# Optimization experiments

Hardware: AMD Instinct MI355X
Metric: run time of the kernel (lower is better)

Reference implementation:

```python
import jax, jax.numpy as jnp
import numpy as np

NEG_SLOPE = 0.01  # torch nn.LeakyReLU default
N_NODES = 100000
N_EDGES = 500000
IN_DIM, OUT_DIM, EF_DIM, EMB_DIM = 128, 128, 64, 256


def leaky_relu(x):
    return jnp.where(x >= 0, x, NEG_SLOPE * x)


def setup_inputs() -> dict:
    key = jax.random.key(0)
    ks = jax.random.split(key, 8)
    s = 0.05
    nf = jax.random.normal(ks[0], (N_NODES, IN_DIM), dtype=jnp.float32)
    ef = jax.random.normal(ks[1], (N_EDGES, EF_DIM), dtype=jnp.float32)
    src = jax.random.randint(ks[2], (N_EDGES,), 0, N_NODES, dtype=jnp.int32)
    dst = jax.random.randint(ks[3], (N_EDGES,), 0, N_NODES, dtype=jnp.int32)
    # Linear weights stored as (in, out); y = x @ W. No biases (bias=False).
    We1 = jax.random.normal(ks[4], (2 * IN_DIM + EF_DIM, EMB_DIM), dtype=jnp.float32) * s
    We2 = jax.random.normal(ks[5], (EMB_DIM, OUT_DIM), dtype=jnp.float32) * s
    Wn1 = jax.random.normal(ks[6], (IN_DIM + OUT_DIM, EMB_DIM), dtype=jnp.float32) * s
    Wn2 = jax.random.normal(ks[7], (EMB_DIM, OUT_DIM), dtype=jnp.float32) * s
    return {"nf": nf, "ef": ef, "src": src, "dst": dst,
            "We1": We1, "We2": We2, "Wn1": Wn1, "Wn2": Wn2}


def reference(nf, ef, src, dst, We1, We2, Wn1, Wn2):
    # Symmetrize: add reversed edges carrying the same edge features.
    src_full = jnp.concatenate([src, dst])            # [2E]
    dst_full = jnp.concatenate([dst, src])            # [2E]
    ef_full = jnp.concatenate([ef, ef], axis=0)       # [2E, ef_dim]

    # message_func: MLP over [src_nf | dst_nf | ef]
    edge_in = jnp.concatenate([nf[src_full], nf[dst_full], ef_full], axis=-1)  # [2E, 2*in+ef]
    msg = leaky_relu(edge_in @ We1) @ We2              # [2E, out]

    # reduce_func: sum messages per destination node (zeros for isolated nodes)
    red = jax.ops.segment_sum(msg, dst_full, num_segments=nf.shape[0])  # [N, out]

    # apply_node_func: MLP over [nf | red_msg]
    node_in = jnp.concatenate([nf, red], axis=-1)      # [N, in+out]
    out_nf = leaky_relu(node_in @ Wn1) @ Wn2           # [N, out]
    return out_nf
```

## Files before the change

### kernel.cpp

```cpp
#include <hip/hip_runtime.h>
#include <hip/hip_bf16.h>
#include <string.h>


using f32x4  = __attribute__((ext_vector_type(4))) float;
using bf16x8 = __attribute__((ext_vector_type(8))) short;

#define LROW 72
#define CROW 132

__device__ __forceinline__ float lrelu(float x) { return x >= 0.f ? x : 0.01f * x; }

__device__ __forceinline__ ushort f2bf(float f) {
    union { float f; unsigned u; } v; v.f = f;
    unsigned u = v.u;
    return (ushort)((u + 0x7fffu + ((u >> 16) & 1u)) >> 16);
}
__device__ __forceinline__ float bf2f(ushort u) {
    union { unsigned u; float f; } v; v.u = ((unsigned)u) << 16; return v.f;
}

__device__ __forceinline__ void atomic_pk_add_bf16(void* addr, unsigned val) {
    asm volatile("global_atomic_pk_add_bf16 %0, %1, off" : : "v"(addr), "v"(val) : "memory");
}

__global__ __launch_bounds__(256) void gemm_bf16(
    const ushort* __restrict__ X1, int K1,
    const ushort* __restrict__ X2, int K2,
    const ushort* __restrict__ Wt,
    void* __restrict__ out, int Nw, int Mstore, int flags)
{
    __shared__ ushort Xs[128 * LROW];
    __shared__ ushort Ws[128 * LROW];

    const int K    = K1 + K2;
    const int tid  = threadIdx.x;
    const int lane = tid & 63;
    const int wv   = tid >> 6;
    const int wm   = wv >> 1, wn = wv & 1;
    const int row0 = blockIdx.x * 128;
    const int col0 = blockIdx.y * 128;

    f32x4 acc[4][4] = {};

    for (int k0 = 0; k0 < K; k0 += 64) {
        const ushort* Xsrc; int kloc, ksz;
        if (k0 < K1) { Xsrc = X1; kloc = k0;      ksz = K1; }
        else         { Xsrc = X2; kloc = k0 - K1; ksz = K2; }

        const int r_  = tid >> 3;
        const int kk  = (tid & 7) * 8;
        uint4 xv[4], wvv[4];
        #pragma unroll
        for (int p = 0; p < 4; ++p) {
            int r = p * 32 + r_;
            xv[p]  = *reinterpret_cast<const uint4*>(Xsrc + (size_t)(row0 + r) * ksz + kloc + kk);
            wvv[p] = *reinterpret_cast<const uint4*>(Wt   + (size_t)(col0 + r) * K   + k0   + kk);
        }
        __syncthreads();
        #pragma unroll
        for (int p = 0; p < 4; ++p) {
            int r = p * 32 + r_;
            *reinterpret_cast<uint4*>(&Xs[r * LROW + kk]) = xv[p];
            *reinterpret_cast<uint4*>(&Ws[r * LROW + kk]) = wvv[p];
        }
        __syncthreads();

        #pragma unroll
        for (int ks = 0; ks < 2; ++ks) {
            bf16x8 af[4], bfr[4];
            #pragma unroll
            for (int i = 0; i < 4; ++i) {
                int mrow = wm * 64 + i * 16 + (lane & 15);
                af[i]  = *reinterpret_cast<const bf16x8*>(&Xs[mrow * LROW + ks * 32 + (lane >> 4) * 8]);
                int ncol = wn * 64 + i * 16 + (lane & 15);
                bfr[i] = *reinterpret_cast<const bf16x8*>(&Ws[ncol * LROW + ks * 32 + (lane >> 4) * 8]);
            }
            #pragma unroll
            for (int i = 0; i < 4; ++i)
                #pragma unroll
                for (int j = 0; j < 4; ++j)
                    acc[i][j] = __builtin_amdgcn_mfma_f32_16x16x32_bf16(af[i], bfr[j], acc[i][j], 0, 0, 0);
        }
    }

    #pragma unroll
    for (int i = 0; i < 4; ++i) {
        int gr0 = row0 + wm * 64 + i * 16 + ((lane >> 4) << 2);
        #pragma unroll
        for (int j = 0; j < 4; ++j) {
            int gc = col0 + wn * 64 + j * 16 + (lane & 15);
            #pragma unroll
            for (int r = 0; r < 4; ++r) {
                int gr = gr0 + r;
                if (gr >= Mstore) continue;
                float v = acc[i][j][r];
                if (flags & 1) v = lrelu(v);
                if (flags & 2) ((ushort*)out)[(size_t)gr * Nw + gc] = f2bf(v);
                else           ((float*) out)[(size_t)gr * Nw + gc] = v;
            }
        }
    }
}

__global__ __launch_bounds__(256) void edge_fused(
    const ushort* __restrict__ efb,
    const ushort* __restrict__ Wet,
    const ushort* __restrict__ AB,
    const int* __restrict__ src, const int* __restrict__ dst,
    ushort* __restrict__ H,
    int E)
{
    __shared__ ushort lds[128 * LROW * 2];
    __shared__ int sd[256];

    const int tid  = threadIdx.x;
    const int lane = tid & 63;
    const int wv   = tid >> 6;
    const int wm   = wv >> 1, wn = wv & 1;
    const int bid  = blockIdx.x;
    const int eb   = (bid >> 1) * 128;
    const int col0 = (bid & 1) * 128;

    ushort* Xs = lds;
    ushort* Ws = lds + 128 * LROW;

    const int r_ = tid >> 3;
    const int kk = (tid & 7) * 8;
    uint4 xv[4], wvv[4];
    #pragma unroll
    for (int p = 0; p < 4; ++p) {
        int r = p * 32 + r_;
        xv[p]  = *reinterpret_cast<const uint4*>(efb + (size_t)(eb + r) * 64 + kk);
        wvv[p] = *reinterpret_cast<const uint4*>(Wet + (size_t)(col0 + r) * 64 + kk);
    }
    if (tid < 128) sd[tid] = (eb + tid < E)         ? src[eb + tid]         : -1;
    else           sd[tid] = (eb + (tid - 128) < E) ? dst[eb + (tid - 128)] : -1;
    #pragma unroll
    for (int p = 0; p < 4; ++p) {
        int r = p * 32 + r_;
        *reinterpret_cast<uint4*>(&Xs[r * LROW + kk]) = xv[p];
        *reinterpret_cast<uint4*>(&Ws[r * LROW + kk]) = wvv[p];
    }
    __syncthreads();

    f32x4 acc[4][4] = {};
    #pragma unroll
    for (int ks = 0; ks < 2; ++ks) {
        bf16x8 af[4], bfr[4];
        #pragma unroll
        for (int i = 0; i < 4; ++i) {
            int mrow = wm * 64 + i * 16 + (lane & 15);
            af[i]  = *reinterpret_cast<const bf16x8*>(&Xs[mrow * LROW + ks * 32 + (lane >> 4) * 8]);
            int ncol = wn * 64 + i * 16 + (lane & 15);
            bfr[i] = *reinterpret_cast<const bf16x8*>(&Ws[ncol * LROW + ks * 32 + (lane >> 4) * 8]);
        }
        #pragma unroll
        for (int i = 0; i < 4; ++i)
            #pragma unroll
            for (int j = 0; j < 4; ++j)
                acc[i][j] = __builtin_amdgcn_mfma_f32_16x16x32_bf16(af[i], bfr[j], acc[i][j], 0, 0, 0);
    }
    __syncthreads();

    ushort* Cs = lds;
    #pragma unroll
    for (int i = 0; i < 4; ++i) {
        int er0 = wm * 64 + i * 16 + ((lane >> 4) << 2);
        #pragma unroll
        for (int j = 0; j < 4; ++j) {
            int fc = wn * 64 + j * 16 + (lane & 15);
            #pragma unroll
            for (int r = 0; r < 4; ++r)
                Cs[(er0 + r) * CROW + fc] = f2bf(acc[i][j][r]);
        }
    }
    __syncthreads();

    const int jj = lane * 2;
    const ushort* ABj = AB + col0 + jj;
    ushort* Hj = H + col0 + jj;
    for (int p = 0; p < 32; ++p) {
        int ee = p * 4 + wv;
        int s = sd[ee], d = sd[128 + ee];
        if (s < 0) continue;
        ushort2 cv = *(const ushort2*)(&Cs[ee * CROW + jj]);
        ushort2 as = *(const ushort2*)(ABj + (size_t)s * 512);
        ushort2 bs = *(const ushort2*)(ABj + (size_t)s * 512 + 256);
        ushort2 ad = *(const ushort2*)(ABj + (size_t)d * 512);
        ushort2 bd = *(const ushort2*)(ABj + (size_t)d * 512 + 256);
        float c0 = bf2f(cv.x), c1 = bf2f(cv.y);
        ushort2 mf, mb;
        mf.x = f2bf(lrelu(bf2f(as.x) + bf2f(bd.x) + c0));
        mf.y = f2bf(lrelu(bf2f(as.y) + bf2f(bd.y) + c1));
        mb.x = f2bf(lrelu(bf2f(ad.x) + bf2f(bs.x) + c0));
        mb.y = f2bf(lrelu(bf2f(ad.y) + bf2f(bs.y) + c1));
        unsigned uf, ub;
        memcpy(&uf, &mf, 4); memcpy(&ub, &mb, 4);
        atomic_pk_add_bf16(Hj + (size_t)d * 256, uf);
        atomic_pk_add_bf16(Hj + (size_t)s * 256, ub);
    }
}

__global__ __launch_bounds__(256) void cvt_pad(
    const float* __restrict__ x, ushort* __restrict__ y, size_t n_real, size_t n_pad)
{
    size_t i = ((size_t)blockIdx.x * 256 + threadIdx.x) * 4;
    if (i >= n_pad) return;
    ushort4 o;
    if (i < n_real) {
        float4 v = *(const float4*)(x + i);
        o.x = f2bf(v.x); o.y = f2bf(v.y); o.z = f2bf(v.z); o.w = f2bf(v.w);
    } else { o.x = 0; o.y = 0; o.z = 0; o.w = 0; }
    *(ushort4*)(y + i) = o;
}

__global__ __launch_bounds__(256) void wcvt(
    const float* __restrict__ We1, const float* __restrict__ We2,
    const float* __restrict__ Wn1, const float* __restrict__ Wn2,
    ushort* __restrict__ Wabt, ushort* __restrict__ Wet, ushort* __restrict__ We2t,
    ushort* __restrict__ Wn1t, ushort* __restrict__ Wn2t)
{
    int idx = blockIdx.x * 256 + threadIdx.x;
    switch (blockIdx.y) {
    case 0: if (idx < 256*128) { int n = idx >> 7, k = idx & 127; Wabt[idx]            = f2bf(We1[k * 256 + n]); } break;
    case 1: if (idx < 256*128) { int n = idx >> 7, k = idx & 127; Wabt[32768 + idx]    = f2bf(We1[(128 + k) * 256 + n]); } break;
    case 2: if (idx < 256*64)  { int n = idx >> 6, k = idx & 63;  Wet[idx]             = f2bf(We1[(256 + k) * 256 + n]); } break;
    case 3: if (idx < 128*256) { int n = idx >> 8, k = idx & 255; We2t[idx]            = f2bf(We2[k * 128 + n]); } break;
    case 4: if (idx < 256*256) { int n = idx >> 8, k = idx & 255; Wn1t[idx]            = f2bf(Wn1[k * 256 + n]); } break;
    case 5: if (idx < 128*256) { int n = idx >> 8, k = idx & 255; Wn2t[idx]            = f2bf(Wn2[k * 128 + n]); } break;
    }
}

extern "C" void kernel_launch(void* const* d_in, const int* in_sizes, int n_in,
                              void* d_out, int out_size, void* d_ws, size_t ws_size,
                              hipStream_t stream) {
    const float* nf  = (const float*)d_in[0];
    const float* ef  = (const float*)d_in[1];
    const int*   src = (const int*)d_in[2];
    const int*   dst = (const int*)d_in[3];
    const float* We1 = (const float*)d_in[4];
    const float* We2 = (const float*)d_in[5];
    const float* Wn1 = (const float*)d_in[6];
    const float* Wn2 = (const float*)d_in[7];
    float* out = (float*)d_out;

    const int  N  = in_sizes[0] / 128;
    const int  E  = in_sizes[2];
    const int  Np = (N + 127) & ~127;
    const long Ep = ((long)E + 127) & ~127L;

    char* p = (char*)d_ws;
    auto alloc = [&](size_t bytes) { char* r = p; p += (bytes + 255) & ~(size_t)255; return r; };
    ushort* AB   = (ushort*)alloc((size_t)Np * 512 * 2);
    ushort* H    = (ushort*)alloc((size_t)Np * 256 * 2);
    ushort* nfb  = (ushort*)alloc((size_t)Np * 128 * 2);
    ushort* efb  = (ushort*)alloc((size_t)Ep * 64 * 2);
    ushort* Wabt = (ushort*)alloc(65536 * 2);
    ushort* Wet  = (ushort*)alloc(16384 * 2);
    ushort* We2t = (ushort*)alloc(32768 * 2);
    ushort* Wn1t = (ushort*)alloc(65536 * 2);
    ushort* Wn2t = (ushort*)alloc(32768 * 2);
    ushort* red = AB;
    ushort* hid = AB + (size_t)Np * 128;

    dim3 blk(256);

    wcvt<<<dim3(256, 6), blk, 0, stream>>>(We1, We2, Wn1, Wn2, Wabt, Wet, We2t, Wn1t, Wn2t);
    cvt_pad<<<dim3((unsigned)((size_t)Np * 128 / 1024)), blk, 0, stream>>>(nf, nfb, (size_t)N * 128, (size_t)Np * 128);
    cvt_pad<<<dim3((unsigned)((size_t)Ep * 64 / 1024)), blk, 0, stream>>>(ef, efb, (size_t)E * 64, (size_t)Ep * 64);

    gemm_bf16<<<dim3(Np / 128, 4), blk, 0, stream>>>(nfb, 128, nullptr, 0, Wabt, AB, 512, Np, 2);

    hipMemsetAsync(H, 0, (size_t)Np * 256 * 2, stream);

    edge_fused<<<dim3((unsigned)(Ep / 128 * 2)), blk, 0, stream>>>(
        efb, Wet, AB, src, dst, H, E);

    gemm_bf16<<<dim3(Np / 128, 1), blk, 0, stream>>>(H, 256, nullptr, 0, We2t, red, 128, Np, 2);
    gemm_bf16<<<dim3(Np / 128, 2), blk, 0, stream>>>(nfb, 128, red, 128, Wn1t, hid, 256, Np, 2 | 1);
    gemm_bf16<<<dim3(Np / 128, 1), blk, 0, stream>>>(hid, 256, nullptr, 0, Wn2t, (void*)out, 128, N, 0);
}
```

Before: 962.2 us.

## Bucket edges by destination node block and reduce messages in LDS

Replaces the per-edge kernel that scattered bf16 packed atomics into global H with a binning pass (count, scan, scatter) that groups directed edges by 64-node destination block. A new kernel then processes each block's edges, computes the edge-feature GEMM per bucket, accumulates messages in fp32 shared memory, and writes H once, removing the global memset and atomics. The cost is extra binning kernels with global atomics, a single-block scan, and a duplicated edge-feature GEMM across both directions. Per-bucket work is also uneven, and the edge-feature rows are now gathered straight from global memory.

```diff
diff --git a/kernel.cpp b/kernel.cpp
--- a/kernel.cpp
+++ b/kernel.cpp
@@ -8,6 +8,8 @@
 
 #define LROW 72
 #define CROW 132
+#define BSH  6
+#define BNODES 64
 
 __device__ __forceinline__ float lrelu(float x) { return x >= 0.f ? x : 0.01f * x; }
 
@@ -18,10 +20,6 @@
 }
 __device__ __forceinline__ float bf2f(ushort u) {
     union { unsigned u; float f; } v; v.u = ((unsigned)u) << 16; return v.f;
-}
-
-__device__ __forceinline__ void atomic_pk_add_bf16(void* addr, unsigned val) {
-    asm volatile("global_atomic_pk_add_bf16 %0, %1, off" : : "v"(addr), "v"(val) : "memory");
 }
 
 __global__ __launch_bounds__(256) void gemm_bf16(
@@ -103,102 +101,162 @@
     }
 }
 
-__global__ __launch_bounds__(256) void edge_fused(
+__global__ __launch_bounds__(256) void ebin_count(
+    const int* __restrict__ src, const int* __restrict__ dst,
+    int* __restrict__ cnt, int E, int NB)
+{
+    int i = blockIdx.x * 256 + threadIdx.x;
+    if (i >= E) return;
+    atomicAdd(&cnt[dst[i] >> BSH], 1);
+    atomicAdd(&cnt[NB + (src[i] >> BSH)], 1);
+}
+
+__global__ __launch_bounds__(256) void escan(
+    const int* __restrict__ cnt, int* __restrict__ base, int* __restrict__ cur, int n)
+{
+    __shared__ int ps[256];
+    const int t = threadIdx.x;
+    const int per = (n + 255) / 256;
+    int s = 0;
+    for (int i = 0; i < per; ++i) { int idx = t * per + i; if (idx < n) s += cnt[idx]; }
+    ps[t] = s;
+    __syncthreads();
+    for (int off = 1; off < 256; off <<= 1) {
+        int u = (t >= off) ? ps[t - off] : 0;
+        __syncthreads();
+        ps[t] += u;
+        __syncthreads();
+    }
+    int run = ps[t] - s;
+    for (int i = 0; i < per; ++i) {
+        int idx = t * per + i;
+        if (idx < n) { base[idx] = run; cur[idx] = run; run += cnt[idx]; }
+    }
+    if (t == 255) base[n] = run;
+}
+
+__global__ __launch_bounds__(256) void escatter(
+    const int* __restrict__ src, const int* __restrict__ dst,
+    int* __restrict__ cur, int* __restrict__ perm, int E, int NB)
+{
+    int i = blockIdx.x * 256 + threadIdx.x;
+    if (i >= E) return;
+    int p1 = atomicAdd(&cur[dst[i] >> BSH], 1);       perm[p1] = i;
+    int p2 = atomicAdd(&cur[NB + (src[i] >> BSH)], 1); perm[p2] = i;
+}
+
+__global__ __launch_bounds__(512) void edge_bucket(
     const ushort* __restrict__ efb,
     const ushort* __restrict__ Wet,
     const ushort* __restrict__ AB,
     const int* __restrict__ src, const int* __restrict__ dst,
+    const int* __restrict__ perm, const int* __restrict__ base,
     ushort* __restrict__ H,
-    int E)
-{
-    __shared__ ushort lds[128 * LROW * 2];
-    __shared__ int sd[256];
-
-    const int tid  = threadIdx.x;
-    const int lane = tid & 63;
-    const int wv   = tid >> 6;
-    const int wm   = wv >> 1, wn = wv & 1;
-    const int bid  = blockIdx.x;
-    const int eb   = (bid >> 1) * 128;
-    const int col0 = (bid & 1) * 128;
-
-    ushort* Xs = lds;
-    ushort* Ws = lds + 128 * LROW;
-
-    const int r_ = tid >> 3;
-    const int kk = (tid & 7) * 8;
-    uint4 xv[4], wvv[4];
+    int NB)
+{
+    __shared__ ushort Ws[128 * LROW];
+    __shared__ ushort Cs[BNODES * CROW];
+    __shared__ float  Hs[BNODES * 128];
+    __shared__ int eids[64], ownl[64], othn[64];
+
+    const int tid   = threadIdx.x;
+    const int lane  = tid & 63;
+    const int wv    = tid >> 6;
+    const int wm    = wv >> 1, wn = wv & 1;
+    const int b     = blockIdx.x;
+    const int col0  = blockIdx.y * 128;
+    const int node0 = b << BSH;
+
     #pragma unroll
-    for (int p = 0; p < 4; ++p) {
-        int r = p * 32 + r_;
-        xv[p]  = *reinterpret_cast<const uint4*>(efb + (size_t)(eb + r) * 64 + kk);
-        wvv[p] = *reinterpret_cast<const uint4*>(Wet + (size_t)(col0 + r) * 64 + kk);
-    }
-    if (tid < 128) sd[tid] = (eb + tid < E)         ? src[eb + tid]         : -1;
-    else           sd[tid] = (eb + (tid - 128) < E) ? dst[eb + (tid - 128)] : -1;
-    #pragma unroll
-    for (int p = 0; p < 4; ++p) {
-        int r = p * 32 + r_;
-        *reinterpret_cast<uint4*>(&Xs[r * LROW + kk]) = xv[p];
-        *reinterpret_cast<uint4*>(&Ws[r * LROW + kk]) = wvv[p];
+    for (int i = 0; i < 16; ++i) Hs[tid + i * 512] = 0.f;
+
+    {
+        const int r_ = tid >> 3;
+        const int kk = (tid & 7) * 8;
+        #pragma unroll
+        for (int p = 0; p < 2; ++p) {
+            int r = p * 64 + r_;
+            *reinterpret_cast<uint4*>(&Ws[r * LROW + kk]) =
+                *reinterpret_cast<const uint4*>(Wet + (size_t)(col0 + r) * 64 + kk);
+        }
+    }
+
+    const int d0 = base[b],      d1 = base[b + 1];
+    const int s0 = base[NB + b], s1 = base[NB + b + 1];
+    const int cd = d1 - d0;
+    const int nv = cd + (s1 - s0);
+
+    for (int v0 = 0; v0 < nv; v0 += 64) {
+        __syncthreads();
+        if (tid < 64) {
+            int vid = v0 + tid;
+            int e = 0, own = -1, oth = 0;
+            if (vid < nv) {
+                if (vid < cd) { e = perm[d0 + vid];      own = dst[e]; oth = src[e]; }
+                else          { e = perm[s0 + vid - cd]; own = src[e]; oth = dst[e]; }
+            }
+            eids[tid] = e;
+            ownl[tid] = (own < 0) ? -1 : own - node0;
+            othn[tid] = oth;
+        }
+        __syncthreads();
+
+        f32x4 acc[4] = {};
+        #pragma unroll
+        for (int ks = 0; ks < 2; ++ks) {
+            int mrow = wm * 16 + (lane & 15);
+            int e = eids[mrow];
+            bf16x8 af = *reinterpret_cast<const bf16x8*>(
+                efb + (size_t)e * 64 + ks * 32 + (lane >> 4) * 8);
+            #pragma unroll
+            for (int j = 0; j < 4; ++j) {
+                int ncol = wn * 64 + j * 16 + (lane & 15);
+                bf16x8 bf = *reinterpret_cast<const bf16x8*>(
+                    &Ws[ncol * LROW + ks * 32 + (lane >> 4) * 8]);
+                acc[j] = __builtin_amdgcn_mfma_f32_16x16x32_bf16(af, bf, acc[j], 0, 0, 0);
+            }
+        }
+        {
+            int er0 = wm * 16 + ((lane >> 4) << 2);
+            #pragma unroll
+            for (int j = 0; j < 4; ++j) {
+                int fc = wn * 64 + j * 16 + (lane & 15);
+                #pragma unroll
+                for (int r = 0; r < 4; ++r)
+                    Cs[(er0 + r) * CROW + fc] = f2bf(acc[j][r]);
+            }
+        }
+        __syncthreads();
+
+        const int jj = lane * 2;
+        #pragma unroll
+        for (int p = 0; p < 8; ++p) {
+            int v = p * 8 + wv;
+            int ol = ownl[v];
+            float w = (ol >= 0) ? 1.f : 0.f;
+            ol &= (BNODES - 1);
+            int oth = othn[v];
+            ushort2 av = *(const ushort2*)(AB + (size_t)oth * 512 + col0 + jj);
+            ushort2 bv = *(const ushort2*)(AB + (size_t)(node0 + ol) * 512 + 256 + col0 + jj);
+            ushort2 cv = *(const ushort2*)(&Cs[v * CROW + jj]);
+            float m0 = lrelu(bf2f(av.x) + bf2f(bv.x) + bf2f(cv.x));
+            float m1 = lrelu(bf2f(av.y) + bf2f(bv.y) + bf2f(cv.y));
+            atomicAdd(&Hs[ol * 128 + jj],     w * m0);
+            atomicAdd(&Hs[ol * 128 + jj + 1], w * m1);
+        }
     }
     __syncthreads();
 
-    f32x4 acc[4][4] = {};
-    #pragma unroll
-    for (int ks = 0; ks < 2; ++ks) {
-        bf16x8 af[4], bfr[4];
-        #pragma unroll
-        for (int i = 0; i < 4; ++i) {
-            int mrow = wm * 64 + i * 16 + (lane & 15);
-            af[i]  = *reinterpret_cast<const bf16x8*>(&Xs[mrow * LROW + ks * 32 + (lane >> 4) * 8]);
-            int ncol = wn * 64 + i * 16 + (lane & 15);
-            bfr[i] = *reinterpret_cast<const bf16x8*>(&Ws[ncol * LROW + ks * 32 + (lane >> 4) * 8]);
-        }
-        #pragma unroll
-        for (int i = 0; i < 4; ++i)
-            #pragma unroll
-            for (int j = 0; j < 4; ++j)
-                acc[i][j] = __builtin_amdgcn_mfma_f32_16x16x32_bf16(af[i], bfr[j], acc[i][j], 0, 0, 0);
-    }
-    __syncthreads();
-
-    ushort* Cs = lds;
-    #pragma unroll
-    for (int i = 0; i < 4; ++i) {
-        int er0 = wm * 64 + i * 16 + ((lane >> 4) << 2);
-        #pragma unroll
-        for (int j = 0; j < 4; ++j) {
-            int fc = wn * 64 + j * 16 + (lane & 15);
-            #pragma unroll
-            for (int r = 0; r < 4; ++r)
-                Cs[(er0 + r) * CROW + fc] = f2bf(acc[i][j][r]);
-        }
-    }
-    __syncthreads();
-
-    const int jj = lane * 2;
-    const ushort* ABj = AB + col0 + jj;
-    ushort* Hj = H + col0 + jj;
-    for (int p = 0; p < 32; ++p) {
-        int ee = p * 4 + wv;
-        int s = sd[ee], d = sd[128 + ee];
-        if (s < 0) continue;
-        ushort2 cv = *(const ushort2*)(&Cs[ee * CROW + jj]);
-        ushort2 as = *(const ushort2*)(ABj + (size_t)s * 512);
-        ushort2 bs = *(const ushort2*)(ABj + (size_t)s * 512 + 256);
-        ushort2 ad = *(const ushort2*)(ABj + (size_t)d * 512);
-        ushort2 bd = *(const ushort2*)(ABj + (size_t)d * 512 + 256);
-        float c0 = bf2f(cv.x), c1 = bf2f(cv.y);
-        ushort2 mf, mb;
-        mf.x = f2bf(lrelu(bf2f(as.x) + bf2f(bd.x) + c0));
-        mf.y = f2bf(lrelu(bf2f(as.y) + bf2f(bd.y) + c1));
-        mb.x = f2bf(lrelu(bf2f(ad.x) + bf2f(bs.x) + c0));
-        mb.y = f2bf(lrelu(bf2f(ad.y) + bf2f(bs.y) + c1));
-        unsigned uf, ub;
-        memcpy(&uf, &mf, 4); memcpy(&ub, &mb, 4);
-        atomic_pk_add_bf16(Hj + (size_t)d * 256, uf);
-        atomic_pk_add_bf16(Hj + (size_t)s * 256, ub);
+    {
+        int row = tid >> 3, seg = tid & 7;
+        ushort* dp = H + (size_t)(node0 + row) * 256 + col0 + seg * 16;
+        #pragma unroll
+        for (int q = 0; q < 8; ++q) {
+            ushort2 o;
+            o.x = f2bf(Hs[row * 128 + seg * 16 + q * 2]);
+            o.y = f2bf(Hs[row * 128 + seg * 16 + q * 2 + 1]);
+            *(ushort2*)(dp + q * 2) = o;
+        }
     }
 }
 
@@ -249,33 +307,42 @@
     const int  E  = in_sizes[2];
     const int  Np = (N + 127) & ~127;
     const long Ep = ((long)E + 127) & ~127L;
+    const int  NB = Np >> BSH;
 
     char* p = (char*)d_ws;
     auto alloc = [&](size_t bytes) { char* r = p; p += (bytes + 255) & ~(size_t)255; return r; };
-    ushort* AB   = (ushort*)alloc((size_t)Np * 512 * 2);
-    ushort* H    = (ushort*)alloc((size_t)Np * 256 * 2);
-    ushort* nfb  = (ushort*)alloc((size_t)Np * 128 * 2);
-    ushort* efb  = (ushort*)alloc((size_t)Ep * 64 * 2);
-    ushort* Wabt = (ushort*)alloc(65536 * 2);
-    ushort* Wet  = (ushort*)alloc(16384 * 2);
-    ushort* We2t = (ushort*)alloc(32768 * 2);
-    ushort* Wn1t = (ushort*)alloc(65536 * 2);
-    ushort* Wn2t = (ushort*)alloc(32768 * 2);
+    ushort* AB    = (ushort*)alloc((size_t)Np * 512 * 2);
+    ushort* H     = (ushort*)alloc((size_t)Np * 256 * 2);
+    ushort* nfb   = (ushort*)alloc((size_t)Np * 128 * 2);
+    ushort* efb   = (ushort*)alloc((size_t)Ep * 64 * 2);
+    ushort* Wabt  = (ushort*)alloc(65536 * 2);
+    ushort* Wet   = (ushort*)alloc(16384 * 2);
+    ushort* We2t  = (ushort*)alloc(32768 * 2);
+    ushort* Wn1t  = (ushort*)alloc(65536 * 2);
+    ushort* Wn2t  = (ushort*)alloc(32768 * 2);
+    int*    cnt   = (int*)alloc((size_t)(2 * NB) * 4);
+    int*    basep = (int*)alloc((size_t)(2 * NB + 1) * 4);
+    int*    cur   = (int*)alloc((size_t)(2 * NB) * 4);
+    int*    perm  = (int*)alloc((size_t)2 * E * 4);
     ushort* red = AB;
     ushort* hid = AB + (size_t)Np * 128;
 
     dim3 blk(256);
+    const unsigned egrid = (unsigned)((E + 255) / 256);
 
     wcvt<<<dim3(256, 6), blk, 0, stream>>>(We1, We2, Wn1, Wn2, Wabt, Wet, We2t, Wn1t, Wn2t);
     cvt_pad<<<dim3((unsigned)((size_t)Np * 128 / 1024)), blk, 0, stream>>>(nf, nfb, (size_t)N * 128, (size_t)Np * 128);
     cvt_pad<<<dim3((unsigned)((size_t)Ep * 64 / 1024)), blk, 0, stream>>>(ef, efb, (size_t)E * 64, (size_t)Ep * 64);
 
+    hipMemsetAsync(cnt, 0, (size_t)(2 * NB) * 4, stream);
+    ebin_count<<<dim3(egrid), blk, 0, stream>>>(src, dst, cnt, E, NB);
+    escan<<<dim3(1), blk, 0, stream>>>(cnt, basep, cur, 2 * NB);
+    escatter<<<dim3(egrid), blk, 0, stream>>>(src, dst, cur, perm, E, NB);
+
     gemm_bf16<<<dim3(Np / 128, 4), blk, 0, stream>>>(nfb, 128, nullptr, 0, Wabt, AB, 512, Np, 2);
 
-    hipMemsetAsync(H, 0, (size_t)Np * 256 * 2, stream);
-
-    edge_fused<<<dim3((unsigned)(Ep / 128 * 2)), blk, 0, stream>>>(
-        efb, Wet, AB, src, dst, H, E);
+    edge_bucket<<<dim3(NB, 2), dim3(512), 0, stream>>>(
+        efb, Wet, AB, src, dst, perm, basep, H, NB);
 
     gemm_bf16<<<dim3(Np / 128, 1), blk, 0, stream>>>(H, 256, nullptr, 0, We2t, red, 128, Np, 2);
     gemm_bf16<<<dim3(Np / 128, 2), blk, 0, stream>>>(nfb, 128, red, 128, Wn1t, hid, 256, Np, 2 | 1);
```

Measured after the change: 2.319 ms. 2.41x slower.

## Fuse node-side GEMM chain into one kernel and specialize AB projection GEMM

Applied to the files above, without the earlier changes.

Replaces the three node-side GEMM launches (H·We2, [nf|red]·Wn1 with leaky ReLU, hid·Wn2) with a single per-row-tile kernel. The kernel keeps the reduced messages and hidden activations in LDS instead of writing them to global memory and reading them back. The AB projection GEMM now loads the node tile into LDS once and loops over all four column blocks, reading weights directly from global memory (likely L2-resident) rather than staging them. The cost is high register and LDS use per block, which may lower occupancy, plus uncoalesced weight reads from global memory.

```diff
diff --git a/kernel.cpp b/kernel.cpp
--- a/kernel.cpp
+++ b/kernel.cpp
@@ -8,6 +8,8 @@
 
 #define LROW 72
 #define CROW 132
+#define P128 132
+#define P256 264
 
 __device__ __forceinline__ float lrelu(float x) { return x >= 0.f ? x : 0.01f * x; }
 
@@ -24,80 +26,55 @@
     asm volatile("global_atomic_pk_add_bf16 %0, %1, off" : : "v"(addr), "v"(val) : "memory");
 }
 
-__global__ __launch_bounds__(256) void gemm_bf16(
-    const ushort* __restrict__ X1, int K1,
-    const ushort* __restrict__ X2, int K2,
+__global__ __launch_bounds__(256) void gemm_ab(
+    const ushort* __restrict__ X,
     const ushort* __restrict__ Wt,
-    void* __restrict__ out, int Nw, int Mstore, int flags)
+    ushort* __restrict__ out)
 {
-    __shared__ ushort Xs[128 * LROW];
-    __shared__ ushort Ws[128 * LROW];
-
-    const int K    = K1 + K2;
+    __shared__ ushort Xs[128 * P128];
     const int tid  = threadIdx.x;
     const int lane = tid & 63;
     const int wv   = tid >> 6;
     const int wm   = wv >> 1, wn = wv & 1;
     const int row0 = blockIdx.x * 128;
-    const int col0 = blockIdx.y * 128;
-
-    f32x4 acc[4][4] = {};
-
-    for (int k0 = 0; k0 < K; k0 += 64) {
-        const ushort* Xsrc; int kloc, ksz;
-        if (k0 < K1) { Xsrc = X1; kloc = k0;      ksz = K1; }
-        else         { Xsrc = X2; kloc = k0 - K1; ksz = K2; }
-
-        const int r_  = tid >> 3;
-        const int kk  = (tid & 7) * 8;
-        uint4 xv[4], wvv[4];
-        #pragma unroll
-        for (int p = 0; p < 4; ++p) {
-            int r = p * 32 + r_;
-            xv[p]  = *reinterpret_cast<const uint4*>(Xsrc + (size_t)(row0 + r) * ksz + kloc + kk);
-            wvv[p] = *reinterpret_cast<const uint4*>(Wt   + (size_t)(col0 + r) * K   + k0   + kk);
-        }
-        __syncthreads();
-        #pragma unroll
-        for (int p = 0; p < 4; ++p) {
-            int r = p * 32 + r_;
-            *reinterpret_cast<uint4*>(&Xs[r * LROW + kk]) = xv[p];
-            *reinterpret_cast<uint4*>(&Ws[r * LROW + kk]) = wvv[p];
-        }
-        __syncthreads();
-
-        #pragma unroll
-        for (int ks = 0; ks < 2; ++ks) {
-            bf16x8 af[4], bfr[4];
+
+    #pragma unroll
+    for (int q = 0; q < 8; ++q) {
+        int idx = q * 256 + tid;
+        int r = idx >> 4, c = idx & 15;
+        *reinterpret_cast<uint4*>(&Xs[r * P128 + c * 8]) =
+            *reinterpret_cast<const uint4*>(X + (size_t)(row0 + r) * 128 + c * 8);
+    }
+    __syncthreads();
+
+    const int g8 = (lane >> 4) * 8;
+    for (int cb = 0; cb < 4; ++cb) {
+        f32x4 acc[4][4] = {};
+        #pragma unroll
+        for (int ks = 0; ks < 4; ++ks) {
+            bf16x8 af[4], bf[4];
             #pragma unroll
             for (int i = 0; i < 4; ++i) {
                 int mrow = wm * 64 + i * 16 + (lane & 15);
-                af[i]  = *reinterpret_cast<const bf16x8*>(&Xs[mrow * LROW + ks * 32 + (lane >> 4) * 8]);
-                int ncol = wn * 64 + i * 16 + (lane & 15);
-                bfr[i] = *reinterpret_cast<const bf16x8*>(&Ws[ncol * LROW + ks * 32 + (lane >> 4) * 8]);
+                af[i] = *reinterpret_cast<const bf16x8*>(&Xs[mrow * P128 + ks * 32 + g8]);
+                int nc = cb * 128 + wn * 64 + i * 16 + (lane & 15);
+                bf[i] = *reinterpret_cast<const bf16x8*>(Wt + (size_t)nc * 128 + ks * 32 + g8);
             }
             #pragma unroll
             for (int i = 0; i < 4; ++i)
                 #pragma unroll
                 for (int j = 0; j < 4; ++j)
-                    acc[i][j] = __builtin_amdgcn_mfma_f32_16x16x32_bf16(af[i], bfr[j], acc[i][j], 0, 0, 0);
-        }
-    }
-
-    #pragma unroll
-    for (int i = 0; i < 4; ++i) {
-        int gr0 = row0 + wm * 64 + i * 16 + ((lane >> 4) << 2);
-        #pragma unroll
-        for (int j = 0; j < 4; ++j) {
-            int gc = col0 + wn * 64 + j * 16 + (lane & 15);
-            #pragma unroll
-            for (int r = 0; r < 4; ++r) {
-                int gr = gr0 + r;
-                if (gr >= Mstore) continue;
-                float v = acc[i][j][r];
-                if (flags & 1) v = lrelu(v);
-                if (flags & 2) ((ushort*)out)[(size_t)gr * Nw + gc] = f2bf(v);
-                else           ((float*) out)[(size_t)gr * Nw + gc] = v;
+                    acc[i][j] = __builtin_amdgcn_mfma_f32_16x16x32_bf16(af[i], bf[j], acc[i][j], 0, 0, 0);
+        }
+        #pragma unroll
+        for (int i = 0; i < 4; ++i) {
+            int gr0 = row0 + wm * 64 + i * 16 + ((lane >> 4) << 2);
+            #pragma unroll
+            for (int j = 0; j < 4; ++j) {
+                int gc = cb * 128 + wn * 64 + j * 16 + (lane & 15);
+                #pragma unroll
+                for (int r = 0; r < 4; ++r)
+                    out[(size_t)(gr0 + r) * 512 + gc] = f2bf(acc[i][j][r]);
             }
         }
     }
@@ -202,6 +179,152 @@
     }
 }
 
+__global__ __launch_bounds__(256) void mlp_fused(
+    const ushort* __restrict__ H,
+    const ushort* __restrict__ nfb,
+    const ushort* __restrict__ We2t,
+    const ushort* __restrict__ Wn1t,
+    const ushort* __restrict__ Wn2t,
+    float* __restrict__ out, int Nreal)
+{
+    __shared__ ushort lds[128 * P256];
+    ushort* Hs  = lds;
+    ushort* Rs  = lds;
+    ushort* Ns  = lds + 128 * P128;
+    ushort* Hid = lds;
+
+    const int tid  = threadIdx.x;
+    const int lane = tid & 63;
+    const int wv   = tid >> 6;
+    const int wm   = wv >> 1, wn = wv & 1;
+    const int row0 = blockIdx.x * 128;
+    const int g8   = (lane >> 4) * 8;
+
+    uint4 npre[8];
+    #pragma unroll
+    for (int q = 0; q < 8; ++q) {
+        int idx = q * 256 + tid;
+        int r = idx >> 4, c = idx & 15;
+        npre[q] = *reinterpret_cast<const uint4*>(nfb + (size_t)(row0 + r) * 128 + c * 8);
+    }
+    #pragma unroll
+    for (int q = 0; q < 16; ++q) {
+        int idx = q * 256 + tid;
+        int r = idx >> 5, c = idx & 31;
+        *reinterpret_cast<uint4*>(&Hs[r * P256 + c * 8]) =
+            *reinterpret_cast<const uint4*>(H + (size_t)(row0 + r) * 256 + c * 8);
+    }
+    __syncthreads();
+
+    f32x4 acc[4][4] = {};
+    #pragma unroll
+    for (int ks = 0; ks < 8; ++ks) {
+        bf16x8 af[4], bf[4];
+        #pragma unroll
+        for (int i = 0; i < 4; ++i) {
+            int mrow = wm * 64 + i * 16 + (lane & 15);
+            af[i] = *reinterpret_cast<const bf16x8*>(&Hs[mrow * P256 + ks * 32 + g8]);
+            int nc = wn * 64 + i * 16 + (lane & 15);
+            bf[i] = *reinterpret_cast<const bf16x8*>(We2t + (size_t)nc * 256 + ks * 32 + g8);
+        }
+        #pragma unroll
+        for (int i = 0; i < 4; ++i)
+            #pragma unroll
+            for (int j = 0; j < 4; ++j)
+                acc[i][j] = __builtin_amdgcn_mfma_f32_16x16x32_bf16(af[i], bf[j], acc[i][j], 0, 0, 0);
+    }
+    __syncthreads();
+
+    #pragma unroll
+    for (int i = 0; i < 4; ++i) {
+        int er0 = wm * 64 + i * 16 + ((lane >> 4) << 2);
+        #pragma unroll
+        for (int j = 0; j < 4; ++j) {
+            int fc = wn * 64 + j * 16 + (lane & 15);
+            #pragma unroll
+            for (int r = 0; r < 4; ++r)
+                Rs[(er0 + r) * P128 + fc] = f2bf(acc[i][j][r]);
+        }
+    }
+    #pragma unroll
+    for (int q = 0; q < 8; ++q) {
+        int idx = q * 256 + tid;
+        int r = idx >> 4, c = idx & 15;
+        *reinterpret_cast<uint4*>(&Ns[r * P128 + c * 8]) = npre[q];
+    }
+    __syncthreads();
+
+    f32x4 a2[2][4][4] = {};
+    #pragma unroll
+    for (int cb = 0; cb < 2; ++cb) {
+        #pragma unroll
+        for (int ks = 0; ks < 8; ++ks) {
+            bf16x8 af[4], bf[4];
+            #pragma unroll
+            for (int i = 0; i < 4; ++i) {
+                int mrow = wm * 64 + i * 16 + (lane & 15);
+                af[i] = (ks < 4)
+                    ? *reinterpret_cast<const bf16x8*>(&Ns[mrow * P128 + ks * 32 + g8])
+                    : *reinterpret_cast<const bf16x8*>(&Rs[mrow * P128 + (ks - 4) * 32 + g8]);
+                int nc = cb * 128 + wn * 64 + i * 16 + (lane & 15);
+                bf[i] = *reinterpret_cast<const bf16x8*>(Wn1t + (size_t)nc * 256 + ks * 32 + g8);
+            }
+            #pragma unroll
+            for (int i = 0; i < 4; ++i)
+                #pragma unroll
+                for (int j = 0; j < 4; ++j)
+                    a2[cb][i][j] = __builtin_amdgcn_mfma_f32_16x16x32_bf16(af[i], bf[j], a2[cb][i][j], 0, 0, 0);
+        }
+    }
+    __syncthreads();
+
+    #pragma unroll
+    for (int cb = 0; cb < 2; ++cb)
+        #pragma unroll
+        for (int i = 0; i < 4; ++i) {
+            int er0 = wm * 64 + i * 16 + ((lane >> 4) << 2);
+            #pragma unroll
+            for (int j = 0; j < 4; ++j) {
+                int fc = cb * 128 + wn * 64 + j * 16 + (lane & 15);
+                #pragma unroll
+                for (int r = 0; r < 4; ++r)
+                    Hid[(er0 + r) * P256 + fc] = f2bf(lrelu(a2[cb][i][j][r]));
+            }
+        }
+    __syncthreads();
+
+    f32x4 a3[4][4] = {};
+    #pragma unroll
+    for (int ks = 0; ks < 8; ++ks) {
+        bf16x8 af[4], bf[4];
+        #pragma unroll
+        for (int i = 0; i < 4; ++i) {
+            int mrow = wm * 64 + i * 16 + (lane & 15);
+            af[i] = *reinterpret_cast<const bf16x8*>(&Hid[mrow * P256 + ks * 32 + g8]);
+            int nc = wn * 64 + i * 16 + (lane & 15);
+            bf[i] = *reinterpret_cast<const bf16x8*>(Wn2t + (size_t)nc * 256 + ks * 32 + g8);
+        }
+        #pragma unroll
+        for (int i = 0; i < 4; ++i)
+            #pragma unroll
+            for (int j = 0; j < 4; ++j)
+                a3[i][j] = __builtin_amdgcn_mfma_f32_16x16x32_bf16(af[i], bf[j], a3[i][j], 0, 0, 0);
+    }
+    #pragma unroll
+    for (int i = 0; i < 4; ++i) {
+        int gr0 = row0 + wm * 64 + i * 16 + ((lane >> 4) << 2);
+        #pragma unroll
+        for (int j = 0; j < 4; ++j) {
+            int gc = wn * 64 + j * 16 + (lane & 15);
+            #pragma unroll
+            for (int r = 0; r < 4; ++r) {
+                int gr = gr0 + r;
+                if (gr < Nreal) out[(size_t)gr * 128 + gc] = a3[i][j][r];
+            }
+        }
+    }
+}
+
 __global__ __launch_bounds__(256) void cvt_pad(
     const float* __restrict__ x, ushort* __restrict__ y, size_t n_real, size_t n_pad)
 {
@@ -261,8 +384,6 @@
     ushort* We2t = (ushort*)alloc(32768 * 2);
     ushort* Wn1t = (ushort*)alloc(65536 * 2);
     ushort* Wn2t = (ushort*)alloc(32768 * 2);
-    ushort* red = AB;
-    ushort* hid = AB + (size_t)Np * 128;
 
     dim3 blk(256);
 
@@ -270,14 +391,12 @@
     cvt_pad<<<dim3((unsigned)((size_t)Np * 128 / 1024)), blk, 0, stream>>>(nf, nfb, (size_t)N * 128, (size_t)Np * 128);
     cvt_pad<<<dim3((unsigned)((size_t)Ep * 64 / 1024)), blk, 0, stream>>>(ef, efb, (size_t)E * 64, (size_t)Ep * 64);
 
-    gemm_bf16<<<dim3(Np / 128, 4), blk, 0, stream>>>(nfb, 128, nullptr, 0, Wabt, AB, 512, Np, 2);
+    gemm_ab<<<dim3(Np / 128), blk, 0, stream>>>(nfb, Wabt, AB);
 
     hipMemsetAsync(H, 0, (size_t)Np * 256 * 2, stream);
 
     edge_fused<<<dim3((unsigned)(Ep / 128 * 2)), blk, 0, stream>>>(
         efb, Wet, AB, src, dst, H, E);
 
-    gemm_bf16<<<dim3(Np / 128, 1), blk, 0, stream>>>(H, 256, nullptr, 0, We2t, red, 128, Np, 2);
-    gemm_bf16<<<dim3(Np / 128, 2), blk, 0, stream>>>(nfb, 128, red, 128, Wn1t, hid, 256, Np, 2 | 1);
-    gemm_bf16<<<dim3(Np / 128, 1), blk, 0, stream>>>(hid, 256, nullptr, 0, Wn2t, (void*)out, 128, N, 0);
-}
+    mlp_fused<<<dim3(Np / 128), blk, 0, stream>>>(H, nfb, We2t, Wn1t, Wn2t, out, N);
+}
```

Measured after the change: 830.0 us. -13.7%, faster.
